# Kernel tuning notes

Measured on AMD Instinct MI355X. Metric: run time of the kernel, lower is better.

The kernel has to match this reference:

```python
import jax, jax.numpy as jnp
import numpy as np

ALPHA = 0.2  # LeakyReLU negative slope
NEG = -9e15

def setup_inputs() -> dict:
    key = jax.random.key(0)
    k1, k2, k3, k4 = jax.random.split(key, 4)
    N, F_in, F_out = 8192, 512, 64
    x = jax.random.normal(k1, (N, F_in), dtype=jnp.float32)
    adj_mat = jax.random.randint(k2, (N, N), 0, 2, dtype=jnp.int32)
    w = jax.random.normal(k3, (F_in, F_out), dtype=jnp.float32) * (2.0 / (F_in + F_out)) ** 0.5
    a = jax.random.normal(k4, (2 * F_out, 1), dtype=jnp.float32) * (2.0 / (2 * F_out + 1)) ** 0.5
    return {"x": x, "adj_mat": adj_mat, "w": w, "a": a}

def reference(x, adj_mat, w, a):
    F_out = w.shape[1]
    wh = x @ w                      # [N, F_out]
    # Decompose concat([wh_i, wh_j]) @ a into two rank-1 score vectors (same math)
    a1, a2 = a[:F_out, 0], a[F_out:, 0]
    e = (wh @ a1)[:, None] + (wh @ a2)[None, :]        # [N, N]
    e = jnp.where(e > 0, e, ALPHA * e)                 # leakyrelu
    attn = jnp.where(adj_mat > 0, e, NEG)
    attn = jax.nn.softmax(attn, axis=1)                # dropout p=0 -> identity
    h_prime = attn @ wh                                # [N, F_out]
    return jnp.where(h_prime > 0, h_prime, jnp.expm1(h_prime))  # elu
```

## Files before the change

kernel.cpp:

```cpp
#include <hip/hip_runtime.h>
#include <hip/hip_bf16.h>

#define ALPHA 0.2f
#define NN 8192
#define FIN 512
#define FOUT 64

typedef __attribute__((ext_vector_type(8))) __bf16 bf16x8;
typedef __attribute__((ext_vector_type(4))) float f32x4;

__global__ __launch_bounds__(256) void k_wh(
    const float* __restrict__ x, const float* __restrict__ w,
    const float* __restrict__ a, float* __restrict__ s1,
    float* __restrict__ s2, uint4* __restrict__ packB) {
  __shared__ float xs[128][64];
  __shared__ unsigned short tile[64][68];
  __shared__ float part1[64][4];
  __shared__ float part2[64][4];
  const int t = threadIdx.x;
  const int r = t & 63;
  const int cg = __builtin_amdgcn_readfirstlane(t >> 6);
  const int row0 = blockIdx.x * 64;

  float acc[16];
#pragma unroll
  for (int u = 0; u < 16; u++) acc[u] = 0.f;

  const int srow = t >> 2;
  const int scol = (t & 3) * 32;

  for (int kc = 0; kc < 4; kc++) {
#pragma unroll
    for (int it = 0; it < 8; it++) {
      float4 v = *(const float4*)(x + (size_t)(row0 + srow) * FIN + kc * 128 + scol + it * 4);
      xs[scol + it * 4 + 0][srow] = v.x;
      xs[scol + it * 4 + 1][srow] = v.y;
      xs[scol + it * 4 + 2][srow] = v.z;
      xs[scol + it * 4 + 3][srow] = v.w;
    }
    __syncthreads();
    const float* wp = w + (size_t)kc * 128 * FOUT + cg * 16;
#pragma unroll 4
    for (int kk = 0; kk < 128; kk++) {
      float av = xs[kk][r];
#pragma unroll
      for (int u = 0; u < 16; u++) acc[u] = fmaf(av, wp[kk * 64 + u], acc[u]);
    }
    __syncthreads();
  }

  float p1 = 0.f, p2 = 0.f;
#pragma unroll
  for (int u = 0; u < 16; u++) {
    p1 = fmaf(acc[u], a[cg * 16 + u], p1);
    p2 = fmaf(acc[u], a[FOUT + cg * 16 + u], p2);
  }
  part1[r][cg] = p1;
  part2[r][cg] = p2;

#pragma unroll
  for (int u = 0; u < 16; u++) {
    __bf16 b = (__bf16)acc[u];
    tile[r][cg * 16 + u] = __builtin_bit_cast(unsigned short, b);
  }
  __syncthreads();

  if (t < 64) {
    s1[row0 + t] = part1[t][0] + part1[t][1] + part1[t][2] + part1[t][3];
    s2[row0 + t] = part2[t][0] + part2[t][1] + part2[t][2] + part2[t][3];
  }

  const int lane = t & 63;
  const int cgw = t >> 6;
  const int col = cgw * 16 + (lane & 15);
#pragma unroll
  for (int e = 0; e < 2; e++) {
    const int rloc = e * 32 + ((lane >> 4) * 8);
    bf16x8 v;
#pragma unroll
    for (int s = 0; s < 8; s++)
      v[s] = __builtin_bit_cast(__bf16, tile[rloc + s][col]);
    packB[(size_t)(((row0 >> 5) + e) * 4 + cgw) * 64 + lane] = __builtin_bit_cast(uint4, v);
  }
}

__global__ __launch_bounds__(512) void k_attn(
    const int* __restrict__ adj, const float* __restrict__ s1,
    const float* __restrict__ s2, const uint4* __restrict__ packB,
    float* __restrict__ out) {
  __shared__ float s2s[NN];
  __shared__ float accp[8][16][64];
  __shared__ float lp[8][16];
  __shared__ float wred[8];

  const int t = threadIdx.x;
  const int wv = t >> 6;
  const int lane = t & 63;

  float m = -1e30f;
#pragma unroll
  for (int it = 0; it < 4; it++) {
    int i4 = t + it * 512;
    float4 v = *(const float4*)&s2[i4 * 4];
    *(float4*)&s2s[i4 * 4] = v;
    m = fmaxf(m, fmaxf(fmaxf(v.x, v.y), fmaxf(v.z, v.w)));
  }
#pragma unroll
  for (int off = 32; off; off >>= 1) m = fmaxf(m, __shfl_xor(m, off));
  if (lane == 0) wred[wv] = m;
  __syncthreads();
  float s2max = wred[0];
#pragma unroll
  for (int u = 1; u < 8; u++) s2max = fmaxf(s2max, wred[u]);

  const int m16 = lane & 15;
  const int kb = lane >> 4;
  const int row0 = blockIdx.x * 16;
  const int i = row0 + m16;
  const float s1v = s1[i];
  float sh = s1v + s2max;
  sh = fmaxf(sh, ALPHA * sh);

  f32x4 acc0 = {0.f, 0.f, 0.f, 0.f};
  f32x4 acc1 = {0.f, 0.f, 0.f, 0.f};
  f32x4 acc2 = {0.f, 0.f, 0.f, 0.f};
  f32x4 acc3 = {0.f, 0.f, 0.f, 0.f};
  float lsum = 0.f;

  const int4* adjp = (const int4*)(adj + (size_t)i * NN) + (wv * 256 + kb * 2);
  const uint4* bp = packB + (size_t)(wv * 32) * 256 + lane;
  int jj = wv * 1024 + kb * 8;

  for (int q = 0; q < 32; q++) {
    const int4 A0 = adjp[0];
    const int4 A1 = adjp[1];
    adjp += 8;
    const float4 S0 = *(const float4*)&s2s[jj];
    const float4 S1 = *(const float4*)&s2s[jj + 4];
    jj += 32;
    const uint4 B0 = bp[0];
    const uint4 B1 = bp[64];
    const uint4 B2 = bp[128];
    const uint4 B3 = bp[192];
    bp += 256;

    float sv[8] = {S0.x, S0.y, S0.z, S0.w, S1.x, S1.y, S1.z, S1.w};
    int av[8] = {A0.x, A0.y, A0.z, A0.w, A1.x, A1.y, A1.z, A1.w};
    bf16x8 af;
#pragma unroll
    for (int v = 0; v < 8; v++) {
      float e = s1v + sv[v];
      float lr = fmaxf(e, ALPHA * e);
      float pv = __expf(lr - sh);
      pv = (av[v] > 0) ? pv : 0.f;
      lsum += pv;
      af[v] = (__bf16)pv;
    }
    acc0 = __builtin_amdgcn_mfma_f32_16x16x32_bf16(af, __builtin_bit_cast(bf16x8, B0), acc0, 0, 0, 0);
    acc1 = __builtin_amdgcn_mfma_f32_16x16x32_bf16(af, __builtin_bit_cast(bf16x8, B1), acc1, 0, 0, 0);
    acc2 = __builtin_amdgcn_mfma_f32_16x16x32_bf16(af, __builtin_bit_cast(bf16x8, B2), acc2, 0, 0, 0);
    acc3 = __builtin_amdgcn_mfma_f32_16x16x32_bf16(af, __builtin_bit_cast(bf16x8, B3), acc3, 0, 0, 0);
  }

  lsum += __shfl_xor(lsum, 16);
  lsum += __shfl_xor(lsum, 32);
  if (lane < 16) lp[wv][lane] = lsum;

#pragma unroll
  for (int rg = 0; rg < 4; rg++) {
    accp[wv][kb * 4 + rg][0 * 16 + m16] = acc0[rg];
    accp[wv][kb * 4 + rg][1 * 16 + m16] = acc1[rg];
    accp[wv][kb * 4 + rg][2 * 16 + m16] = acc2[rg];
    accp[wv][kb * 4 + rg][3 * 16 + m16] = acc3[rg];
  }
  __syncthreads();

#pragma unroll
  for (int u = 0; u < 2; u++) {
    int idx = t + u * 512;
    int rr = idx >> 6;
    int cc = idx & 63;
    float s = 0.f, l = 0.f;
#pragma unroll
    for (int wq = 0; wq < 8; wq++) {
      s += accp[wq][rr][cc];
      l += lp[wq][rr];
    }
    float h = s / l;
    out[(size_t)(row0 + rr) * FOUT + cc] = (h > 0.f) ? h : (__expf(h) - 1.f);
  }
}

extern "C" void kernel_launch(void* const* d_in, const int* in_sizes, int n_in,
                              void* d_out, int out_size, void* d_ws, size_t ws_size,
                              hipStream_t stream) {
  const float* x = (const float*)d_in[0];
  const int* adj = (const int*)d_in[1];
  const float* w = (const float*)d_in[2];
  const float* a = (const float*)d_in[3];
  float* out = (float*)d_out;

  char* ws = (char*)d_ws;
  float* s1 = (float*)ws;
  float* s2 = s1 + NN;
  uint4* packB = (uint4*)(ws + 2 * (size_t)NN * 4);

  k_wh<<<dim3(128), dim3(256), 0, stream>>>(x, w, a, s1, s2, packB);
  k_attn<<<dim3(512), dim3(512), 0, stream>>>(adj, s1, s2, packB, out);
}
```

Baseline: 460.9 us.

## Alias attention LDS buffers, prefetch next tile, use exp2 with prescaled scores

The attention kernel overlays the s2 score buffer and the epilogue reduction buffers in one shared-memory union, so LDS per block shrinks from about 65 KB to about 33 KB. It also sets a minimum of 4 blocks per CU in launch bounds, software-prefetches the next iteration's adjacency and packed-B loads, and folds log2(e) into the scores so the inner loop can use a bare exp2. The aim is more resident waves plus better latency hiding on the memory-bound adjacency stream. The occupancy hint and the extra prefetch registers could force spills, and an added barrier now guards reuse of the aliased LDS.

```diff
diff --git a/kernel.cpp b/kernel.cpp
--- a/kernel.cpp
+++ b/kernel.cpp
@@ -5,6 +5,7 @@
 #define NN 8192
 #define FIN 512
 #define FOUT 64
+#define LOG2E 1.4426950408889634f
 
 typedef __attribute__((ext_vector_type(8))) __bf16 bf16x8;
 typedef __attribute__((ext_vector_type(4))) float f32x4;
@@ -84,13 +85,17 @@
   }
 }
 
-__global__ __launch_bounds__(512) void k_attn(
+__global__ __launch_bounds__(512, 4) void k_attn(
     const int* __restrict__ adj, const float* __restrict__ s1,
     const float* __restrict__ s2, const uint4* __restrict__ packB,
     float* __restrict__ out) {
-  __shared__ float s2s[NN];
-  __shared__ float accp[8][16][64];
-  __shared__ float lp[8][16];
+  __shared__ union {
+    float s2s[NN];
+    struct {
+      float accp[8][16][64];
+      float lp[8][16];
+    } ep;
+  } sm;
   __shared__ float wred[8];
 
   const int t = threadIdx.x;
@@ -102,24 +107,25 @@
   for (int it = 0; it < 4; it++) {
     int i4 = t + it * 512;
     float4 v = *(const float4*)&s2[i4 * 4];
-    *(float4*)&s2s[i4 * 4] = v;
+    v.x *= LOG2E; v.y *= LOG2E; v.z *= LOG2E; v.w *= LOG2E;
+    *(float4*)&sm.s2s[i4 * 4] = v;
     m = fmaxf(m, fmaxf(fmaxf(v.x, v.y), fmaxf(v.z, v.w)));
   }
 #pragma unroll
   for (int off = 32; off; off >>= 1) m = fmaxf(m, __shfl_xor(m, off));
   if (lane == 0) wred[wv] = m;
   __syncthreads();
-  float s2max = wred[0];
-#pragma unroll
-  for (int u = 1; u < 8; u++) s2max = fmaxf(s2max, wred[u]);
+  float s2lmax = wred[0];
+#pragma unroll
+  for (int u = 1; u < 8; u++) s2lmax = fmaxf(s2lmax, wred[u]);
 
   const int m16 = lane & 15;
   const int kb = lane >> 4;
   const int row0 = blockIdx.x * 16;
   const int i = row0 + m16;
-  const float s1v = s1[i];
-  float sh = s1v + s2max;
-  sh = fmaxf(sh, ALPHA * sh);
+  const float s1l = s1[i] * LOG2E;
+  float shl = s1l + s2lmax;
+  shl = fmaxf(shl, ALPHA * shl);
 
   f32x4 acc0 = {0.f, 0.f, 0.f, 0.f};
   f32x4 acc1 = {0.f, 0.f, 0.f, 0.f};
@@ -131,27 +137,30 @@
   const uint4* bp = packB + (size_t)(wv * 32) * 256 + lane;
   int jj = wv * 1024 + kb * 8;
 
+  int4 A0 = adjp[0], A1 = adjp[1];
+  uint4 B0 = bp[0], B1 = bp[64], B2 = bp[128], B3 = bp[192];
+
   for (int q = 0; q < 32; q++) {
-    const int4 A0 = adjp[0];
-    const int4 A1 = adjp[1];
     adjp += 8;
-    const float4 S0 = *(const float4*)&s2s[jj];
-    const float4 S1 = *(const float4*)&s2s[jj + 4];
+    bp += 256;
+    int4 nA0, nA1;
+    uint4 nB0, nB1, nB2, nB3;
+    if (q < 31) {
+      nA0 = adjp[0]; nA1 = adjp[1];
+      nB0 = bp[0]; nB1 = bp[64]; nB2 = bp[128]; nB3 = bp[192];
+    }
+    const float4 S0 = *(const float4*)&sm.s2s[jj];
+    const float4 S1 = *(const float4*)&sm.s2s[jj + 4];
     jj += 32;
-    const uint4 B0 = bp[0];
-    const uint4 B1 = bp[64];
-    const uint4 B2 = bp[128];
-    const uint4 B3 = bp[192];
-    bp += 256;
 
     float sv[8] = {S0.x, S0.y, S0.z, S0.w, S1.x, S1.y, S1.z, S1.w};
     int av[8] = {A0.x, A0.y, A0.z, A0.w, A1.x, A1.y, A1.z, A1.w};
     bf16x8 af;
 #pragma unroll
     for (int v = 0; v < 8; v++) {
-      float e = s1v + sv[v];
-      float lr = fmaxf(e, ALPHA * e);
-      float pv = __expf(lr - sh);
+      float el = s1l + sv[v];
+      float lr = fmaxf(el, ALPHA * el);
+      float pv = __builtin_amdgcn_exp2f(lr - shl);
       pv = (av[v] > 0) ? pv : 0.f;
       lsum += pv;
       af[v] = (__bf16)pv;
@@ -160,18 +169,22 @@
     acc1 = __builtin_amdgcn_mfma_f32_16x16x32_bf16(af, __builtin_bit_cast(bf16x8, B1), acc1, 0, 0, 0);
     acc2 = __builtin_amdgcn_mfma_f32_16x16x32_bf16(af, __builtin_bit_cast(bf16x8, B2), acc2, 0, 0, 0);
     acc3 = __builtin_amdgcn_mfma_f32_16x16x32_bf16(af, __builtin_bit_cast(bf16x8, B3), acc3, 0, 0, 0);
+    A0 = nA0; A1 = nA1;
+    B0 = nB0; B1 = nB1; B2 = nB2; B3 = nB3;
   }
 
   lsum += __shfl_xor(lsum, 16);
   lsum += __shfl_xor(lsum, 32);
-  if (lane < 16) lp[wv][lane] = lsum;
-
+
+  __syncthreads();
+
+  if (lane < 16) sm.ep.lp[wv][lane] = lsum;
 #pragma unroll
   for (int rg = 0; rg < 4; rg++) {
-    accp[wv][kb * 4 + rg][0 * 16 + m16] = acc0[rg];
-    accp[wv][kb * 4 + rg][1 * 16 + m16] = acc1[rg];
-    accp[wv][kb * 4 + rg][2 * 16 + m16] = acc2[rg];
-    accp[wv][kb * 4 + rg][3 * 16 + m16] = acc3[rg];
+    sm.ep.accp[wv][kb * 4 + rg][0 * 16 + m16] = acc0[rg];
+    sm.ep.accp[wv][kb * 4 + rg][1 * 16 + m16] = acc1[rg];
+    sm.ep.accp[wv][kb * 4 + rg][2 * 16 + m16] = acc2[rg];
+    sm.ep.accp[wv][kb * 4 + rg][3 * 16 + m16] = acc3[rg];
   }
   __syncthreads();
 
@@ -183,8 +196,8 @@
     float s = 0.f, l = 0.f;
 #pragma unroll
     for (int wq = 0; wq < 8; wq++) {
-      s += accp[wq][rr][cc];
-      l += lp[wq][rr];
+      s += sm.ep.accp[wq][rr][cc];
+      l += sm.ep.lp[wq][rr];
     }
     float h = s / l;
     out[(size_t)(row0 + rr) * FOUT + cc] = (h > 0.f) ? h : (__expf(h) - 1.f);
```

Result: no change. 466.4 us (+1.2%).
